# Performance work log

Hardware: AMD Instinct MI355X
Metric: run time of the kernel (lower is better)

The kernel has to match this reference:

```python
import jax, jax.numpy as jnp
import numpy as np

B, S, H, HEADS = 2, 512, 768, 12
HD = H // HEADS  # head dim 64
LN_EPS = 1e-5


def setup_inputs() -> dict:
    key = jax.random.key(0)
    ks = jax.random.split(key, 8)
    w = lambda k, shape: jax.random.normal(k, shape, dtype=jnp.float32) * 0.02
    return {
        "hidden_states": jax.random.normal(ks[0], (B, S, H), dtype=jnp.float32),
        "attention_mask": jnp.ones((B, S), dtype=jnp.int32),
        "Wp": w(ks[1], (H, H)), "bp": jnp.zeros((H,), jnp.float32),   # input_projection
        "Wq": w(ks[2], (H, H)), "bq": jnp.zeros((H,), jnp.float32),   # MHA q in-proj
        "Wk": w(ks[3], (H, H)), "bk": jnp.zeros((H,), jnp.float32),   # MHA k in-proj
        "We": w(ks[4], (H, H)), "be": jnp.zeros((H,), jnp.float32),   # edge_projection
        "gamma": jnp.ones((H,), jnp.float32), "beta": jnp.zeros((H,), jnp.float32),
    }


def reference(hidden_states, attention_mask, Wp, bp, Wq, bq, Wk, bk, We, be, gamma, beta):
    b, s, _ = hidden_states.shape
    # input projection (dropout = identity at eval)
    node = hidden_states @ Wp.T + bp                                   # [B,S,H]

    # self-attention weights (per-head), key_padding_mask = ~attention_mask
    q = (node @ Wq.T + bq).reshape(b, s, HEADS, HD).transpose(0, 2, 1, 3)
    k = (node @ Wk.T + bk).reshape(b, s, HEADS, HD).transpose(0, 2, 1, 3)
    logits = jnp.einsum("bhqd,bhkd->bhqk", q, k) / jnp.sqrt(jnp.float32(HD))
    pad = (attention_mask == 0)                                        # [B,S] keys to mask
    logits = jnp.where(pad[:, None, None, :], jnp.float32(-1e9), logits)
    attn = jax.nn.softmax(logits, axis=-1)                             # [B,HEADS,S,S]
    avg = attn.mean(axis=1)                                            # [B,S,S]

    # top-k sparsification: k = S // 2 neighbors per node
    ktop = s // 2
    _, idx = jax.lax.top_k(avg, ktop)                                  # [B,S,ktop]
    idx = jnp.sort(idx, axis=-1)  # torch.where emits dst in ascending order per src row
    scores = jnp.take_along_axis(avg, idx, axis=-1)                    # [B,S,ktop]

    # edge index with per-batch node offsets (all-ones mask -> every row kept)
    src = jnp.broadcast_to(jnp.arange(s)[None, :, None], (b, s, ktop))
    offset = (jnp.arange(b) * s)[:, None, None]
    edge_index = jnp.stack([(src + offset).reshape(-1),
                            (idx + offset).reshape(-1)], axis=0)       # [2, B*S*ktop]

    # edge_attr: zeros with col 0 = attn score, then Linear  ==  score * We[:,0] + be
    edge_attr = scores.reshape(-1)[:, None] * We[:, 0][None, :] + be   # [E, H]

    # final layer norm on node features
    mu = node.mean(axis=-1, keepdims=True)
    var = ((node - mu) ** 2).mean(axis=-1, keepdims=True)
    node_features = (node - mu) * jax.lax.rsqrt(var + LN_EPS) * gamma + beta

    return node_features, edge_index, edge_attr
```

## Files before the change

### kernel.cpp

```cpp
#include <hip/hip_runtime.h>

#define HH 768
#define SS 512
#define NB 2
#define NHEADS 12
#define KTOP 256
#define ETOT (NB*SS*KTOP)
#define LN_EPS 1e-5f

#define EI_OFF 786432L
#define EA_OFF 1310720L
#define PSZ    786432L

#define FMA16(a,b) \
    acc[0][0]=fmaf(a.x,b.x,acc[0][0]); acc[0][1]=fmaf(a.x,b.y,acc[0][1]); \
    acc[0][2]=fmaf(a.x,b.z,acc[0][2]); acc[0][3]=fmaf(a.x,b.w,acc[0][3]); \
    acc[1][0]=fmaf(a.y,b.x,acc[1][0]); acc[1][1]=fmaf(a.y,b.y,acc[1][1]); \
    acc[1][2]=fmaf(a.y,b.z,acc[1][2]); acc[1][3]=fmaf(a.y,b.w,acc[1][3]); \
    acc[2][0]=fmaf(a.z,b.x,acc[2][0]); acc[2][1]=fmaf(a.z,b.y,acc[2][1]); \
    acc[2][2]=fmaf(a.z,b.z,acc[2][2]); acc[2][3]=fmaf(a.z,b.w,acc[2][3]); \
    acc[3][0]=fmaf(a.w,b.x,acc[3][0]); acc[3][1]=fmaf(a.w,b.y,acc[3][1]); \
    acc[3][2]=fmaf(a.w,b.z,acc[3][2]); acc[3][3]=fmaf(a.w,b.w,acc[3][3]);

#define STORE_TILE(DST, V0, V1) \
    (DST)[sc4*4+0][srow]    = (V0).x; (DST)[sc4*4+1][srow]    = (V0).y; \
    (DST)[sc4*4+2][srow]    = (V0).z; (DST)[sc4*4+3][srow]    = (V0).w; \
    (DST)[sc4*4+0][srow+32] = (V1).x; (DST)[sc4*4+1][srow+32] = (V1).y; \
    (DST)[sc4*4+2][srow+32] = (V1).z; (DST)[sc4*4+3][srow+32] = (V1).w;

__device__ __forceinline__ float4 f4sum(const float* __restrict__ p0,
                                        const float* __restrict__ p1,
                                        const float* __restrict__ b,
                                        long off, int bcol)
{
    const float4 x = *(const float4*)(p0 + off);
    const float4 y = *(const float4*)(p1 + off);
    const float4 z = *(const float4*)(b + bcol);
    float4 r;
    r.x = x.x + y.x + z.x; r.y = x.y + y.y + z.y;
    r.z = x.z + y.z + z.z; r.w = x.w + y.w + z.w;
    return r;
}

__global__ __launch_bounds__(256, 3) void gemm_sk1(
    const float* __restrict__ A, const float* __restrict__ W,
    float* __restrict__ P)
{
    __shared__ float As[2][32][68];
    __shared__ float Ws[2][32][68];
    const int tid = threadIdx.x;
    const int tm = tid >> 4, tn = tid & 15;
    const int m0 = blockIdx.y * 64, n0 = blockIdx.x * 64;
    const int kh = blockIdx.z;
    const int srow = tid >> 3, sc4 = tid & 7;
    const int kbeg = kh * 384;

    const float* Ar0 = A + (long)(m0 + srow) * HH + kbeg + sc4 * 4;
    const float* Ar1 = Ar0 + 32 * HH;
    const float* Wr0 = W + (long)(n0 + srow) * HH + kbeg + sc4 * 4;
    const float* Wr1 = Wr0 + 32 * HH;

    float4 pa0 = *(const float4*)Ar0, pa1 = *(const float4*)Ar1;
    float4 pw0 = *(const float4*)Wr0, pw1 = *(const float4*)Wr1;

    float acc[4][4] = {};
    for (int kt = 0; kt < 12; ++kt) {
        const int cur = kt & 1;
        STORE_TILE(As[cur], pa0, pa1);
        STORE_TILE(Ws[cur], pw0, pw1);
        __syncthreads();
        if (kt < 11) {
            const int off = (kt + 1) * 32;
            pa0 = *(const float4*)(Ar0 + off);
            pa1 = *(const float4*)(Ar1 + off);
            pw0 = *(const float4*)(Wr0 + off);
            pw1 = *(const float4*)(Wr1 + off);
        }
        #pragma unroll
        for (int k = 0; k < 32; ++k) {
            const float4 a = *(const float4*)&As[cur][k][tm*4];
            const float4 b = *(const float4*)&Ws[cur][k][tn*4];
            FMA16(a, b)
        }
    }

    float* C = P + (long)kh * PSZ + (long)m0 * HH + n0;
    #pragma unroll
    for (int i = 0; i < 4; ++i) {
        float4 r;
        r.x = acc[i][0]; r.y = acc[i][1]; r.z = acc[i][2]; r.w = acc[i][3];
        *(float4*)(C + (long)(tm*4 + i) * HH + tn * 4) = r;
    }
}

__global__ __launch_bounds__(256, 3) void gemm_sk2(
    const float* __restrict__ P, const float* __restrict__ bp,
    const float* __restrict__ Wq, const float* __restrict__ Wk,
    float* __restrict__ QKP,
    const float* __restrict__ gamma, const float* __restrict__ beta,
    float* __restrict__ lnout)
{
    __shared__ float As[2][32][68];
    __shared__ float Ws[2][32][68];
    __shared__ float rs_[4], rq_[4];
    const int tid = threadIdx.x;

    if (blockIdx.z == 4) {
        const int fb = blockIdx.y * 12 + blockIdx.x;
        const int t  = tid;
        for (int row = fb; row < NB * SS; row += 192) {
            const float* x0 = P + (long)row * HH;
            const float* x1 = x0 + PSZ;
            const float v0 = x0[t]       + x1[t]       + bp[t];
            const float v1 = x0[t + 256] + x1[t + 256] + bp[t + 256];
            const float v2 = x0[t + 512] + x1[t + 512] + bp[t + 512];
            float s  = v0 + v1 + v2;
            float sq = v0 * v0 + v1 * v1 + v2 * v2;
            #pragma unroll
            for (int o = 32; o >= 1; o >>= 1) {
                s  += __shfl_xor(s, o);
                sq += __shfl_xor(sq, o);
            }
            if ((t & 63) == 0) { rs_[t >> 6] = s; rq_[t >> 6] = sq; }
            __syncthreads();
            const float S = rs_[0] + rs_[1] + rs_[2] + rs_[3];
            const float Q = rq_[0] + rq_[1] + rq_[2] + rq_[3];
            const float mu  = S * (1.f / HH);
            const float var = Q * (1.f / HH) - mu * mu;
            const float inv = rsqrtf(var + LN_EPS);
            float* o = lnout + (long)row * HH;
            o[t]       = (v0 - mu) * inv * gamma[t]       + beta[t];
            o[t + 256] = (v1 - mu) * inv * gamma[t + 256] + beta[t + 256];
            o[t + 512] = (v2 - mu) * inv * gamma[t + 512] + beta[t + 512];
            __syncthreads();
        }
        return;
    }

    const int tm = tid >> 4, tn = tid & 15;
    const int m0 = blockIdx.y * 64, n0 = blockIdx.x * 64;
    const int sel = blockIdx.z >> 1, kh = blockIdx.z & 1;
    const float* W = sel ? Wk : Wq;
    const int srow = tid >> 3, sc4 = tid & 7;
    const int kbeg = kh * 384;

    const float* P1 = P + PSZ;
    const long aoff0 = (long)(m0 + srow) * HH + kbeg + sc4 * 4;
    const long aoff1 = aoff0 + 32 * HH;
    const int  bcol  = kbeg + sc4 * 4;
    const float* Wr0 = W + (long)(n0 + srow) * HH + kbeg + sc4 * 4;
    const float* Wr1 = Wr0 + 32 * HH;

    float4 pa0 = f4sum(P, P1, bp, aoff0, bcol);
    float4 pa1 = f4sum(P, P1, bp, aoff1, bcol);
    float4 pw0 = *(const float4*)Wr0;
    float4 pw1 = *(const float4*)Wr1;

    float acc[4][4] = {};
    for (int kt = 0; kt < 12; ++kt) {
        const int cur = kt & 1;
        STORE_TILE(As[cur], pa0, pa1);
        STORE_TILE(Ws[cur], pw0, pw1);
        __syncthreads();
        if (kt < 11) {
            const int off = (kt + 1) * 32;
            pa0 = f4sum(P, P1, bp, aoff0 + off, bcol + off);
            pa1 = f4sum(P, P1, bp, aoff1 + off, bcol + off);
            pw0 = *(const float4*)(Wr0 + off);
            pw1 = *(const float4*)(Wr1 + off);
        }
        #pragma unroll
        for (int k = 0; k < 32; ++k) {
            const float4 a = *(const float4*)&As[cur][k][tm*4];
            const float4 b = *(const float4*)&Ws[cur][k][tn*4];
            FMA16(a, b)
        }
    }

    float* C = QKP + ((long)sel * 2 + kh) * PSZ + (long)m0 * HH + n0;
    #pragma unroll
    for (int i = 0; i < 4; ++i) {
        float4 r;
        r.x = acc[i][0]; r.y = acc[i][1]; r.z = acc[i][2]; r.w = acc[i][3];
        *(float4*)(C + (long)(tm*4 + i) * HH + tn * 4) = r;
    }
}

__global__ __launch_bounds__(256, 3) void gemm_qk2(
    const float* __restrict__ QKP, const float* __restrict__ bq,
    const float* __restrict__ bk, float* __restrict__ logits)
{
    __shared__ float As[2][32][68];
    __shared__ float Ws[2][32][68];
    const int tid = threadIdx.x;
    const int tm = tid >> 4, tn = tid & 15;
    const int m0 = blockIdx.y * 64, n0 = blockIdx.x * 64;
    const int z = blockIdx.z, bz = z / NHEADS, hz = z - bz * NHEADS;
    const int srow = tid >> 3, sc4 = tid & 7;

    const float* q0 = QKP;
    const float* q1 = QKP + PSZ;
    const float* k0 = QKP + 2 * PSZ;
    const float* k1 = QKP + 3 * PSZ;

    const long rbase = (long)bz * SS * HH + hz * 64;
    const long aoff0 = rbase + (long)(m0 + srow) * HH + sc4 * 4;
    const long aoff1 = aoff0 + 32 * HH;
    const long woff0 = rbase + (long)(n0 + srow) * HH + sc4 * 4;
    const long woff1 = woff0 + 32 * HH;
    const int  bcol  = hz * 64 + sc4 * 4;

    float4 pa0 = f4sum(q0, q1, bq, aoff0, bcol);
    float4 pa1 = f4sum(q0, q1, bq, aoff1, bcol);
    float4 pw0 = f4sum(k0, k1, bk, woff0, bcol);
    float4 pw1 = f4sum(k0, k1, bk, woff1, bcol);

    float acc[4][4] = {};
    for (int kt = 0; kt < 2; ++kt) {
        const int cur = kt & 1;
        STORE_TILE(As[cur], pa0, pa1);
        STORE_TILE(Ws[cur], pw0, pw1);
        __syncthreads();
        if (kt == 0) {
            pa0 = f4sum(q0, q1, bq, aoff0 + 32, bcol + 32);
            pa1 = f4sum(q0, q1, bq, aoff1 + 32, bcol + 32);
            pw0 = f4sum(k0, k1, bk, woff0 + 32, bcol + 32);
            pw1 = f4sum(k0, k1, bk, woff1 + 32, bcol + 32);
        }
        #pragma unroll
        for (int k = 0; k < 32; ++k) {
            const float4 a = *(const float4*)&As[cur][k][tm*4];
            const float4 b = *(const float4*)&Ws[cur][k][tn*4];
            FMA16(a, b)
        }
    }

    float* C = logits + (long)z * SS * SS;
    #pragma unroll
    for (int i = 0; i < 4; ++i) {
        float4 r;
        r.x = acc[i][0] * 0.125f;
        r.y = acc[i][1] * 0.125f;
        r.z = acc[i][2] * 0.125f;
        r.w = acc[i][3] * 0.125f;
        *(float4*)(C + (long)(m0 + tm*4 + i) * SS + n0 + tn * 4) = r;
    }
}

__global__ __launch_bounds__(256) void attn_edge(
    const float* __restrict__ logits,
    const int*   __restrict__ mask,
    const float* __restrict__ We, const float* __restrict__ be,
    float* __restrict__ ei,
    float* __restrict__ ea)
{
    const int row = blockIdx.x;
    const int b   = row >> 9;
    const int qi  = row & 511;
    const int t   = threadIdx.x;
    const int wid = t >> 6, lane = t & 63;

    __shared__ float red[NHEADS][4];
    __shared__ unsigned long long keys[SS];
    __shared__ float4 wt[192], bt[192];
    __shared__ unsigned long long mskS[8];
    __shared__ float ssel[KTOP];

    if (t < 192) {
        float4 w;
        w.x = We[(long)(4 * t + 0) * HH];
        w.y = We[(long)(4 * t + 1) * HH];
        w.z = We[(long)(4 * t + 2) * HH];
        w.w = We[(long)(4 * t + 3) * HH];
        wt[t] = w;
        bt[t] = *(const float4*)(be + 4 * t);
    }

    const bool m0 = mask[b * SS + t] != 0;
    const bool m1 = mask[b * SS + t + 256] != 0;

    const float* basep = logits + ((long)b * NHEADS * SS + qi) * SS;

    float x0[NHEADS], x1[NHEADS];
    #pragma unroll
    for (int h = 0; h < NHEADS; ++h) {
        const float* lr = basep + (long)h * SS * SS;
        x0[h] = lr[t];
        x1[h] = lr[t + 256];
    }

    #pragma unroll
    for (int h = 0; h < NHEADS; ++h) {
        x0[h] = m0 ? __expf(x0[h]) : 0.f;
        x1[h] = m1 ? __expf(x1[h]) : 0.f;
        float s = x0[h] + x1[h];
        #pragma unroll
        for (int o = 32; o >= 1; o >>= 1) s += __shfl_xor(s, o);
        if (lane == 0) red[h][wid] = s;
    }
    __syncthreads();

    float a0 = 0.f, a1 = 0.f;
    #pragma unroll
    for (int h = 0; h < NHEADS; ++h) {
        const float rs = 1.0f / (red[h][0] + red[h][1] + red[h][2] + red[h][3]);
        a0 = fmaf(x0[h], rs, a0);
        a1 = fmaf(x1[h], rs, a1);
    }
    a0 *= (1.f / NHEADS);
    a1 *= (1.f / NHEADS);

    const unsigned long long k0 =
        ((unsigned long long)__float_as_uint(a0) << 32) | (unsigned)(SS - 1 - t);
    const unsigned long long k1 =
        ((unsigned long long)__float_as_uint(a1) << 32) | (unsigned)(SS - 1 - (t + 256));
    keys[t]       = k0;
    keys[t + 256] = k1;
    __syncthreads();

    int r0 = 0, r1 = 0;
    #pragma unroll 8
    for (int j = 0; j < SS; ++j) {
        const unsigned long long kj = keys[j];
        r0 += (kj > k0);
        r1 += (kj > k1);
    }
    const bool sel0 = (r0 < KTOP);
    const bool sel1 = (r1 < KTOP);

    const unsigned long long mm0 = __ballot(sel0);
    const unsigned long long mm1 = __ballot(sel1);
    if (lane == 0) { mskS[wid] = mm0; mskS[4 + wid] = mm1; }
    __syncthreads();
    int cum[8]; int acc = 0;
    #pragma unroll
    for (int i = 0; i < 8; ++i) { cum[i] = acc; acc += __popcll(mskS[i]); }
    const unsigned long long lt = lane ? ((1ull << lane) - 1ull) : 0ull;
    const int p0 = cum[wid]     + __popcll(mskS[wid]     & lt);
    const int p1 = cum[4 + wid] + __popcll(mskS[4 + wid] & lt);

    const float srcv = (float)(b * SS + qi);
    const long  base_e = (long)row * KTOP;
    if (sel0) {
        ei[base_e + p0]        = srcv;
        ei[ETOT + base_e + p0] = (float)(b * SS + t);
        ssel[p0]               = a0;
    }
    if (sel1) {
        ei[base_e + p1]        = srcv;
        ei[ETOT + base_e + p1] = (float)(b * SS + t + 256);
        ssel[p1]               = a1;
    }
    __syncthreads();

    const int cA = t % 192, cB = (t + 64) % 192, cC = (t + 128) % 192;
    const float4 wA = wt[cA], bA = bt[cA];
    const float4 wB = wt[cB], bB = bt[cB];
    const float4 wC = wt[cC], bC = bt[cC];

    float4* dst = (float4*)(ea + base_e * HH);
    for (int m = 0; m < 64; ++m) {
        const int e_lo = m * 4;
        {
            const int e = e_lo + (t >= 192 ? 1 : 0);
            const float s = ssel[e];
            float4 r;
            r.x = fmaf(s, wA.x, bA.x); r.y = fmaf(s, wA.y, bA.y);
            r.z = fmaf(s, wA.z, bA.z); r.w = fmaf(s, wA.w, bA.w);
            dst[(3*m + 0) * 256 + t] = r;
        }
        {
            const int e = e_lo + 1 + (t >= 128 ? 1 : 0);
            const float s = ssel[e];
            float4 r;
            r.x = fmaf(s, wB.x, bB.x); r.y = fmaf(s, wB.y, bB.y);
            r.z = fmaf(s, wB.z, bB.z); r.w = fmaf(s, wB.w, bB.w);
            dst[(3*m + 1) * 256 + t] = r;
        }
        {
            const int e = e_lo + 2 + (t >= 64 ? 1 : 0);
            const float s = ssel[e];
            float4 r;
            r.x = fmaf(s, wC.x, bC.x); r.y = fmaf(s, wC.y, bC.y);
            r.z = fmaf(s, wC.z, bC.z); r.w = fmaf(s, wC.w, bC.w);
            dst[(3*m + 2) * 256 + t] = r;
        }
    }
}

extern "C" void kernel_launch(void* const* d_in, const int* in_sizes, int n_in,
                              void* d_out, int out_size, void* d_ws, size_t ws_size,
                              hipStream_t stream)
{
    const float* hidden = (const float*)d_in[0];
    const int*   mask   = (const int*)  d_in[1];
    const float* Wp = (const float*)d_in[2];
    const float* bp = (const float*)d_in[3];
    const float* Wq = (const float*)d_in[4];
    const float* bq = (const float*)d_in[5];
    const float* Wk = (const float*)d_in[6];
    const float* bk = (const float*)d_in[7];
    const float* We = (const float*)d_in[8];
    const float* be = (const float*)d_in[9];
    const float* gamma = (const float*)d_in[10];
    const float* beta  = (const float*)d_in[11];

    float* out = (float*)d_out;
    float* ws  = (float*)d_ws;

    float* logits = ws;
    float* pn     = out + EA_OFF;
    float* qkp    = out + EA_OFF + 2*PSZ;

    const dim3 blk(256);

    gemm_sk1<<<dim3(12, 16, 2), blk, 0, stream>>>(hidden, Wp, pn);
    gemm_sk2<<<dim3(12, 16, 5), blk, 0, stream>>>(pn, bp, Wq, Wk, qkp,
                                                  gamma, beta, out);
    gemm_qk2<<<dim3(8, 8, NB * NHEADS), blk, 0, stream>>>(qkp, bq, bk, logits);
    attn_edge<<<dim3(NB * SS), blk, 0, stream>>>(logits, mask, We, be,
                                                 out + EI_OFF, out + EA_OFF);
}
```

Baseline: 245.9 us.

## Split attention top-k and edge_attr writing into separate kernels

Splits the fused attn_edge kernel in two. attn_topk computes the averaged softmax and the top-k selection per row, then writes the selected scores to a workspace buffer. A new edge_writer kernel with 2048 blocks streams the large edge_attr output using a flat, coalesced float4 layout. This decouples the bandwidth-heavy output write from the 1024-block selection kernel, at the cost of an extra launch and a small round trip of scores through global memory.

```diff
diff --git a/kernel.cpp b/kernel.cpp
--- a/kernel.cpp
+++ b/kernel.cpp
@@ -247,12 +247,11 @@
     }
 }
 
-__global__ __launch_bounds__(256) void attn_edge(
+__global__ __launch_bounds__(256) void attn_topk(
     const float* __restrict__ logits,
     const int*   __restrict__ mask,
-    const float* __restrict__ We, const float* __restrict__ be,
     float* __restrict__ ei,
-    float* __restrict__ ea)
+    float* __restrict__ sscore)
 {
     const int row = blockIdx.x;
     const int b   = row >> 9;
@@ -262,10 +261,94 @@
 
     __shared__ float red[NHEADS][4];
     __shared__ unsigned long long keys[SS];
-    __shared__ float4 wt[192], bt[192];
     __shared__ unsigned long long mskS[8];
-    __shared__ float ssel[KTOP];
-
+
+    const bool m0 = mask[b * SS + t] != 0;
+    const bool m1 = mask[b * SS + t + 256] != 0;
+
+    const float* basep = logits + ((long)b * NHEADS * SS + qi) * SS;
+
+    float x0[NHEADS], x1[NHEADS];
+    #pragma unroll
+    for (int h = 0; h < NHEADS; ++h) {
+        const float* lr = basep + (long)h * SS * SS;
+        x0[h] = lr[t];
+        x1[h] = lr[t + 256];
+    }
+
+    #pragma unroll
+    for (int h = 0; h < NHEADS; ++h) {
+        x0[h] = m0 ? __expf(x0[h]) : 0.f;
+        x1[h] = m1 ? __expf(x1[h]) : 0.f;
+        float s = x0[h] + x1[h];
+        #pragma unroll
+        for (int o = 32; o >= 1; o >>= 1) s += __shfl_xor(s, o);
+        if (lane == 0) red[h][wid] = s;
+    }
+    __syncthreads();
+
+    float a0 = 0.f, a1 = 0.f;
+    #pragma unroll
+    for (int h = 0; h < NHEADS; ++h) {
+        const float rs = 1.0f / (red[h][0] + red[h][1] + red[h][2] + red[h][3]);
+        a0 = fmaf(x0[h], rs, a0);
+        a1 = fmaf(x1[h], rs, a1);
+    }
+    a0 *= (1.f / NHEADS);
+    a1 *= (1.f / NHEADS);
+
+    const unsigned long long k0 =
+        ((unsigned long long)__float_as_uint(a0) << 32) | (unsigned)(SS - 1 - t);
+    const unsigned long long k1 =
+        ((unsigned long long)__float_as_uint(a1) << 32) | (unsigned)(SS - 1 - (t + 256));
+    keys[t]       = k0;
+    keys[t + 256] = k1;
+    __syncthreads();
+
+    int r0 = 0, r1 = 0;
+    #pragma unroll 8
+    for (int j = 0; j < SS; ++j) {
+        const unsigned long long kj = keys[j];
+        r0 += (kj > k0);
+        r1 += (kj > k1);
+    }
+    const bool sel0 = (r0 < KTOP);
+    const bool sel1 = (r1 < KTOP);
+
+    const unsigned long long mm0 = __ballot(sel0);
+    const unsigned long long mm1 = __ballot(sel1);
+    if (lane == 0) { mskS[wid] = mm0; mskS[4 + wid] = mm1; }
+    __syncthreads();
+    int cum[8]; int acc = 0;
+    #pragma unroll
+    for (int i = 0; i < 8; ++i) { cum[i] = acc; acc += __popcll(mskS[i]); }
+    const unsigned long long lt = lane ? ((1ull << lane) - 1ull) : 0ull;
+    const int p0 = cum[wid]     + __popcll(mskS[wid]     & lt);
+    const int p1 = cum[4 + wid] + __popcll(mskS[4 + wid] & lt);
+
+    const float srcv = (float)(b * SS + qi);
+    const long  base_e = (long)row * KTOP;
+    if (sel0) {
+        ei[base_e + p0]        = srcv;
+        ei[ETOT + base_e + p0] = (float)(b * SS + t);
+        sscore[base_e + p0]    = a0;
+    }
+    if (sel1) {
+        ei[base_e + p1]        = srcv;
+        ei[ETOT + base_e + p1] = (float)(b * SS + t + 256);
+        sscore[base_e + p1]    = a1;
+    }
+}
+
+#define EA_STR  524288L
+
+__global__ __launch_bounds__(256) void edge_writer(
+    const float* __restrict__ scores, const float* __restrict__ We,
+    const float* __restrict__ be, float* __restrict__ out)
+{
+    __shared__ float4 wt[192];
+    __shared__ float4 bt[192];
+    const int t = threadIdx.x;
     if (t < 192) {
         float4 w;
         w.x = We[(long)(4 * t + 0) * HH];
@@ -275,116 +358,37 @@
         wt[t] = w;
         bt[t] = *(const float4*)(be + 4 * t);
     }
-
-    const bool m0 = mask[b * SS + t] != 0;
-    const bool m1 = mask[b * SS + t + 256] != 0;
-
-    const float* basep = logits + ((long)b * NHEADS * SS + qi) * SS;
-
-    float x0[NHEADS], x1[NHEADS];
-    #pragma unroll
-    for (int h = 0; h < NHEADS; ++h) {
-        const float* lr = basep + (long)h * SS * SS;
-        x0[h] = lr[t];
-        x1[h] = lr[t + 256];
-    }
-
-    #pragma unroll
-    for (int h = 0; h < NHEADS; ++h) {
-        x0[h] = m0 ? __expf(x0[h]) : 0.f;
-        x1[h] = m1 ? __expf(x1[h]) : 0.f;
-        float s = x0[h] + x1[h];
-        #pragma unroll
-        for (int o = 32; o >= 1; o >>= 1) s += __shfl_xor(s, o);
-        if (lane == 0) red[h][wid] = s;
-    }
     __syncthreads();
 
-    float a0 = 0.f, a1 = 0.f;
-    #pragma unroll
-    for (int h = 0; h < NHEADS; ++h) {
-        const float rs = 1.0f / (red[h][0] + red[h][1] + red[h][2] + red[h][3]);
-        a0 = fmaf(x0[h], rs, a0);
-        a1 = fmaf(x1[h], rs, a1);
-    }
-    a0 *= (1.f / NHEADS);
-    a1 *= (1.f / NHEADS);
-
-    const unsigned long long k0 =
-        ((unsigned long long)__float_as_uint(a0) << 32) | (unsigned)(SS - 1 - t);
-    const unsigned long long k1 =
-        ((unsigned long long)__float_as_uint(a1) << 32) | (unsigned)(SS - 1 - (t + 256));
-    keys[t]       = k0;
-    keys[t + 256] = k1;
-    __syncthreads();
-
-    int r0 = 0, r1 = 0;
-    #pragma unroll 8
-    for (int j = 0; j < SS; ++j) {
-        const unsigned long long kj = keys[j];
-        r0 += (kj > k0);
-        r1 += (kj > k1);
-    }
-    const bool sel0 = (r0 < KTOP);
-    const bool sel1 = (r1 < KTOP);
-
-    const unsigned long long mm0 = __ballot(sel0);
-    const unsigned long long mm1 = __ballot(sel1);
-    if (lane == 0) { mskS[wid] = mm0; mskS[4 + wid] = mm1; }
-    __syncthreads();
-    int cum[8]; int acc = 0;
-    #pragma unroll
-    for (int i = 0; i < 8; ++i) { cum[i] = acc; acc += __popcll(mskS[i]); }
-    const unsigned long long lt = lane ? ((1ull << lane) - 1ull) : 0ull;
-    const int p0 = cum[wid]     + __popcll(mskS[wid]     & lt);
-    const int p1 = cum[4 + wid] + __popcll(mskS[4 + wid] & lt);
-
-    const float srcv = (float)(b * SS + qi);
-    const long  base_e = (long)row * KTOP;
-    if (sel0) {
-        ei[base_e + p0]        = srcv;
-        ei[ETOT + base_e + p0] = (float)(b * SS + t);
-        ssel[p0]               = a0;
-    }
-    if (sel1) {
-        ei[base_e + p1]        = srcv;
-        ei[ETOT + base_e + p1] = (float)(b * SS + t + 256);
-        ssel[p1]               = a1;
-    }
-    __syncthreads();
-
-    const int cA = t % 192, cB = (t + 64) % 192, cC = (t + 128) % 192;
-    const float4 wA = wt[cA], bA = bt[cA];
-    const float4 wB = wt[cB], bB = bt[cB];
-    const float4 wC = wt[cC], bC = bt[cC];
-
-    float4* dst = (float4*)(ea + base_e * HH);
-    for (int m = 0; m < 64; ++m) {
-        const int e_lo = m * 4;
-        {
-            const int e = e_lo + (t >= 192 ? 1 : 0);
-            const float s = ssel[e];
-            float4 r;
-            r.x = fmaf(s, wA.x, bA.x); r.y = fmaf(s, wA.y, bA.y);
-            r.z = fmaf(s, wA.z, bA.z); r.w = fmaf(s, wA.w, bA.w);
-            dst[(3*m + 0) * 256 + t] = r;
-        }
-        {
-            const int e = e_lo + 1 + (t >= 128 ? 1 : 0);
-            const float s = ssel[e];
-            float4 r;
-            r.x = fmaf(s, wB.x, bB.x); r.y = fmaf(s, wB.y, bB.y);
-            r.z = fmaf(s, wB.z, bB.z); r.w = fmaf(s, wB.w, bB.w);
-            dst[(3*m + 1) * 256 + t] = r;
-        }
-        {
-            const int e = e_lo + 2 + (t >= 64 ? 1 : 0);
-            const float s = ssel[e];
-            float4 r;
-            r.x = fmaf(s, wC.x, bC.x); r.y = fmaf(s, wC.y, bC.y);
-            r.z = fmaf(s, wC.z, bC.z); r.w = fmaf(s, wC.w, bC.w);
-            dst[(3*m + 2) * 256 + t] = r;
-        }
+    long f0 = (long)blockIdx.x * 256 + t;
+    long f1 = f0 + EA_STR;
+    long f2 = f1 + EA_STR;
+    int  e0 = (int)(f0 / 192), c0 = (int)(f0 % 192);
+    int  e1 = (int)(f1 / 192), c1 = (int)(f1 % 192);
+    int  e2 = (int)(f2 / 192), c2 = (int)(f2 % 192);
+
+    const float4 wA = wt[c0], bA = bt[c0];
+    const float4 wB = wt[c1], bB = bt[c1];
+    const float4 wC = wt[c2], bC = bt[c2];
+
+    float4* o4 = (float4*)out;
+    #pragma unroll 2
+    for (int m = 0; m < 32; ++m) {
+        const float s0 = scores[e0];
+        const float s1 = scores[e1];
+        const float s2 = scores[e2];
+        float4 r0, r1, r2;
+        r0.x = fmaf(s0, wA.x, bA.x); r0.y = fmaf(s0, wA.y, bA.y);
+        r0.z = fmaf(s0, wA.z, bA.z); r0.w = fmaf(s0, wA.w, bA.w);
+        r1.x = fmaf(s1, wB.x, bB.x); r1.y = fmaf(s1, wB.y, bB.y);
+        r1.z = fmaf(s1, wB.z, bB.z); r1.w = fmaf(s1, wB.w, bB.w);
+        r2.x = fmaf(s2, wC.x, bC.x); r2.y = fmaf(s2, wC.y, bC.y);
+        r2.z = fmaf(s2, wC.z, bC.z); r2.w = fmaf(s2, wC.w, bC.w);
+        o4[f0] = r0;
+        o4[f1] = r1;
+        o4[f2] = r2;
+        e0 += 8192; e1 += 8192; e2 += 8192;
+        f0 += 3 * EA_STR; f1 += 3 * EA_STR; f2 += 3 * EA_STR;
     }
 }
 
@@ -409,6 +413,7 @@
     float* ws  = (float*)d_ws;
 
     float* logits = ws;
+    float* sscore = ws + 6291456;
     float* pn     = out + EA_OFF;
     float* qkp    = out + EA_OFF + 2*PSZ;
 
@@ -418,6 +423,6 @@
     gemm_sk2<<<dim3(12, 16, 5), blk, 0, stream>>>(pn, bp, Wq, Wk, qkp,
                                                   gamma, beta, out);
     gemm_qk2<<<dim3(8, 8, NB * NHEADS), blk, 0, stream>>>(qkp, bq, bk, logits);
-    attn_edge<<<dim3(NB * SS), blk, 0, stream>>>(logits, mask, We, be,
-                                                 out + EI_OFF, out + EA_OFF);
-}
+    attn_topk<<<dim3(NB * SS), blk, 0, stream>>>(logits, mask, out + EI_OFF, sscore);
+    edge_writer<<<dim3(2048), blk, 0, stream>>>(sscore, We, be, out + EA_OFF);
+}
```

Result: slower. 274.9 us (+11.8%).
